# Performance work log

Hardware: AMD Instinct MI355X
Metric: run time of the kernel (lower is better)

## Reference

```python
import jax, jax.numpy as jnp
import numpy as np

N = 100000   # nodes
E = 1600000  # edges (edge_index1)
F_IN = 53    # num_features_xd
D1 = 128     # output_dim1
D2 = 64      # output_dim2
G = 512      # graphs in batch


def setup_inputs() -> dict:
    key = jax.random.key(0)
    ks = jax.random.split(key, 16)
    kaiming = lambda k, fi, fo: jax.random.normal(k, (fi, fo), jnp.float32) * np.float32(np.sqrt(2.0 / fi))
    glorot = lambda k, fi, fo: jax.random.normal(k, (fi, fo), jnp.float32) * np.float32(np.sqrt(1.0 / fi))
    return {
        "x": jax.random.normal(ks[0], (N, F_IN), jnp.float32),
        "edge_inter": jax.random.randint(ks[1], (2, E), 0, N),
        "edge_intra": jax.random.randint(ks[2], (2, E), 0, N),
        "batch": jnp.sort(jax.random.randint(ks[3], (N,), 0, G)),
        "num_graphs": G,
        "w1": kaiming(ks[4], F_IN, D1), "b1": jnp.zeros((D1,), jnp.float32),
        "w2": kaiming(ks[5], D1, D2), "b2": jnp.zeros((D2,), jnp.float32),
        "gat_w": glorot(ks[6], D2, D2),
        "att_src": jax.random.normal(ks[7], (D2,), jnp.float32) * 0.1,
        "att_dst": jax.random.normal(ks[8], (D2,), jnp.float32) * 0.1,
        "gat_b": jnp.zeros((D2,), jnp.float32),
        "gcn_w": glorot(ks[9], D2, 2 * D2), "gcn_b": jnp.zeros((2 * D2,), jnp.float32),
        "fc1_w": glorot(ks[10], 2 * D2, 512), "fc1_b": jnp.zeros((512,), jnp.float32),
        "fc2_w": glorot(ks[11], 512, 256), "fc2_b": jnp.zeros((256,), jnp.float32),
        "out_w": glorot(ks[12], 256, 1), "out_b": jnp.zeros((1,), jnp.float32),
    }


def reference(x, edge_inter, edge_intra, batch, num_graphs,
              w1, b1, w2, b2, gat_w, att_src, att_dst, gat_b,
              gcn_w, gcn_b, fc1_w, fc1_b, fc2_w, fc2_b, out_w, out_b):
    n = x.shape[0]
    # node_embed: two dense layers + relu
    h = jax.nn.relu(x @ w1 + b1)
    h = jax.nn.relu(h @ w2 + b2)

    # add self-loops (PyG default for GATConv and GCNConv)
    loops = jnp.arange(n)
    src = jnp.concatenate([edge_inter[0], loops])  # message source j
    dst = jnp.concatenate([edge_inter[1], loops])  # message target i

    # ---- GATConv (heads=1): gather -> score -> edge softmax -> scatter ----
    hp = h @ gat_w                           # [N, D2]
    a_s = hp @ att_src                       # [N]
    a_d = hp @ att_dst                       # [N]
    e = jax.nn.leaky_relu(a_s[src] + a_d[dst], negative_slope=0.2)  # [E+N]
    emax = jax.ops.segment_max(e, dst, num_segments=n)
    ee = jnp.exp(e - emax[dst])
    denom = jax.ops.segment_sum(ee, dst, num_segments=n)
    alpha = ee / denom[dst]                  # edge softmax per target node
    h = jax.ops.segment_sum(alpha[:, None] * hp[src], dst, num_segments=n) + gat_b
    h = jax.nn.relu(h)

    # ---- GCNConv: symmetric-normalized sparse aggregation ----
    hw = h @ gcn_w                           # [N, 2*D2]
    deg = jax.ops.segment_sum(jnp.ones_like(e), dst, num_segments=n)
    d_inv = jnp.where(deg > 0, deg ** -0.5, 0.0)
    norm = d_inv[src] * d_inv[dst]           # [E+N]
    h = jax.ops.segment_sum(norm[:, None] * hw[src], dst, num_segments=n) + gcn_b
    h = jax.nn.relu(h)

    # ---- global max pool over graphs ----
    g = jax.ops.segment_max(h, batch, num_segments=num_graphs)
    g = jnp.maximum(g, 0.0)  # guard empty segments (-inf); h >= 0 after relu

    # ---- MLP head (dropout is identity in eval mode) ----
    z = jax.nn.relu(g @ fc1_w + fc1_b)
    z = jax.nn.relu(z @ fc2_w + fc2_b)
    return z @ out_w + out_b
```

## Files before the change

### kernel.cpp

```cpp
#include <hip/hip_runtime.h>
#include <hip/hip_bf16.h>

#define F_IN 53
#define D1   128
#define D2   64
#define D3   128
#define H1SZ 512
#define H2SZ 256

#define BUKSZ   256
#define BUKMAX  512
#define CAP     5120
#define PART_CH 4096

__global__ void k_vecproj(const float* __restrict__ gat_w,
                          const float* __restrict__ att_src,
                          const float* __restrict__ att_dst,
                          float* __restrict__ v_src, float* __restrict__ v_dst) {
    int k = threadIdx.x;
    float as = 0.f, ad = 0.f;
    #pragma unroll
    for (int c = 0; c < D2; ++c) {
        float w = gat_w[k * D2 + c];
        as = fmaf(w, att_src[c], as);
        ad = fmaf(w, att_dst[c], ad);
    }
    v_src[k] = as;
    v_dst[k] = ad;
}

__global__ __launch_bounds__(256) void k_fused(const float* __restrict__ x,
                                               const float* __restrict__ w1,
                                               const float* __restrict__ b1,
                                               const float* __restrict__ w2,
                                               const float* __restrict__ b2,
                                               const float* __restrict__ gat_w,
                                               const float* __restrict__ v_src,
                                               const float* __restrict__ v_dst,
                                               float* __restrict__ hp,
                                               float* __restrict__ a_s,
                                               float* __restrict__ a_d,
                                               const int* __restrict__ ei,
                                               int* __restrict__ gcount,
                                               int2* __restrict__ tmp,
                                               const int* __restrict__ batch,
                                               int* __restrict__ gstart,
                                               int N, int E, int NBUK, int G,
                                               int embB, int partB) {
    __shared__ __align__(16) union {
        struct { float xs[32][56]; float h1s[32][D1]; float h2s[32][D2]; } e;
        int hist[BUKMAX];
    } sm;
    int tid = threadIdx.x;
    int bid = blockIdx.x;

    if (bid >= embB) {
        if (bid < embB + partB) {
            for (int i = tid; i < NBUK; i += 256) sm.hist[i] = 0;
            __syncthreads();
            int k0 = (bid - embB) * PART_CH;
            int ss[16], dd[16];
            #pragma unroll
            for (int i = 0; i < 16; ++i) {
                int k = k0 + i * 256 + tid;
                if (k < E) {
                    ss[i] = ei[k];
                    dd[i] = ei[E + k];
                    atomicAdd(&sm.hist[dd[i] >> 8], 1);
                } else {
                    dd[i] = -1;
                }
            }
            __syncthreads();
            for (int b = tid; b < NBUK; b += 256) {
                int c = sm.hist[b];
                if (c > 0) sm.hist[b] = b * CAP + atomicAdd(&gcount[b], c);
            }
            __syncthreads();
            #pragma unroll
            for (int i = 0; i < 16; ++i) {
                if (dd[i] >= 0) {
                    int b = dd[i] >> 8;
                    int pos = atomicAdd(&sm.hist[b], 1);
                    if (pos < (b + 1) * CAP) tmp[pos] = make_int2(ss[i], dd[i]);
                }
            }
        } else {
            int n = (bid - embB - partB) * 256 + tid;
            if (n < N) {
                int b = batch[n];
                if (n == 0) {
                    for (int g = 0; g <= b; ++g) gstart[g] = 0;
                } else {
                    int pb = batch[n - 1];
                    for (int g = pb + 1; g <= b; ++g) gstart[g] = n;
                }
                if (n == N - 1) {
                    for (int g = b + 1; g <= G; ++g) gstart[g] = N;
                }
            }
        }
        return;
    }

    int n0 = bid * 32;
    for (int i = tid; i < 32 * F_IN; i += 256) {
        int node = i / F_IN, kk = i - node * F_IN;
        sm.e.xs[node][kk] = x[(size_t)n0 * F_IN + i];
    }
    __syncthreads();
    int c = tid & 63, grp = tid >> 6;
    int nb = grp * 8;
    {
        float acc0[8], acc1[8];
        float bb0 = b1[c], bb1 = b1[c + 64];
        #pragma unroll
        for (int j = 0; j < 8; ++j) { acc0[j] = bb0; acc1[j] = bb1; }
        #pragma unroll 1
        for (int kc = 0; kc < 13; ++kc) {
            int k4 = kc * 4;
            float wa0 = w1[(k4 + 0) * D1 + c];
            float wa1 = w1[(k4 + 1) * D1 + c];
            float wa2 = w1[(k4 + 2) * D1 + c];
            float wa3 = w1[(k4 + 3) * D1 + c];
            float wb0 = w1[(k4 + 0) * D1 + c + 64];
            float wb1 = w1[(k4 + 1) * D1 + c + 64];
            float wb2 = w1[(k4 + 2) * D1 + c + 64];
            float wb3 = w1[(k4 + 3) * D1 + c + 64];
            #pragma unroll
            for (int j = 0; j < 8; ++j) {
                float4 xv = *reinterpret_cast<const float4*>(&sm.e.xs[nb + j][k4]);
                acc0[j] = fmaf(xv.x, wa0, acc0[j]);
                acc0[j] = fmaf(xv.y, wa1, acc0[j]);
                acc0[j] = fmaf(xv.z, wa2, acc0[j]);
                acc0[j] = fmaf(xv.w, wa3, acc0[j]);
                acc1[j] = fmaf(xv.x, wb0, acc1[j]);
                acc1[j] = fmaf(xv.y, wb1, acc1[j]);
                acc1[j] = fmaf(xv.z, wb2, acc1[j]);
                acc1[j] = fmaf(xv.w, wb3, acc1[j]);
            }
        }
        {
            float wa = w1[52 * D1 + c], wb = w1[52 * D1 + c + 64];
            #pragma unroll
            for (int j = 0; j < 8; ++j) {
                float xv = sm.e.xs[nb + j][52];
                acc0[j] = fmaf(xv, wa, acc0[j]);
                acc1[j] = fmaf(xv, wb, acc1[j]);
            }
        }
        #pragma unroll
        for (int j = 0; j < 8; ++j) {
            sm.e.h1s[nb + j][c]      = fmaxf(acc0[j], 0.f);
            sm.e.h1s[nb + j][c + 64] = fmaxf(acc1[j], 0.f);
        }
    }
    float h2v[8];
    {
        float bb = b2[c];
        #pragma unroll
        for (int j = 0; j < 8; ++j) h2v[j] = bb;
        #pragma unroll 1
        for (int kc = 0; kc < 32; ++kc) {
            int k4 = kc * 4;
            float w0 = w2[(k4 + 0) * D2 + c];
            float w1v = w2[(k4 + 1) * D2 + c];
            float w2v = w2[(k4 + 2) * D2 + c];
            float w3v = w2[(k4 + 3) * D2 + c];
            #pragma unroll
            for (int j = 0; j < 8; ++j) {
                float4 hv = *reinterpret_cast<const float4*>(&sm.e.h1s[nb + j][k4]);
                h2v[j] = fmaf(hv.x, w0, h2v[j]);
                h2v[j] = fmaf(hv.y, w1v, h2v[j]);
                h2v[j] = fmaf(hv.z, w2v, h2v[j]);
                h2v[j] = fmaf(hv.w, w3v, h2v[j]);
            }
        }
        #pragma unroll
        for (int j = 0; j < 8; ++j) {
            float v = fmaxf(h2v[j], 0.f);
            h2v[j] = v;
            sm.e.h2s[nb + j][c] = v;
        }
    }
    {
        float vs = v_src[c], vd = v_dst[c];
        #pragma unroll
        for (int j = 0; j < 8; ++j) {
            float ps = h2v[j] * vs, pd = h2v[j] * vd;
            #pragma unroll
            for (int off = 32; off; off >>= 1) {
                ps += __shfl_down(ps, off);
                pd += __shfl_down(pd, off);
            }
            if (c == 0) { int n = n0 + nb + j; a_s[n] = ps; a_d[n] = pd; }
        }
    }
    {
        float acc[8];
        #pragma unroll
        for (int j = 0; j < 8; ++j) acc[j] = 0.f;
        #pragma unroll 1
        for (int kc = 0; kc < 16; ++kc) {
            int k4 = kc * 4;
            float w0 = gat_w[(k4 + 0) * D2 + c];
            float w1v = gat_w[(k4 + 1) * D2 + c];
            float w2v = gat_w[(k4 + 2) * D2 + c];
            float w3v = gat_w[(k4 + 3) * D2 + c];
            #pragma unroll
            for (int j = 0; j < 8; ++j) {
                float4 hv = *reinterpret_cast<const float4*>(&sm.e.h2s[nb + j][k4]);
                acc[j] = fmaf(hv.x, w0, acc[j]);
                acc[j] = fmaf(hv.y, w1v, acc[j]);
                acc[j] = fmaf(hv.z, w2v, acc[j]);
                acc[j] = fmaf(hv.w, w3v, acc[j]);
            }
        }
        #pragma unroll
        for (int j = 0; j < 8; ++j)
            hp[(size_t)(n0 + nb + j) * D2 + c] = acc[j];
    }
}

__global__ __launch_bounds__(256) void k_build(const int2* __restrict__ tmp,
                                               const int* __restrict__ gcount,
                                               int* __restrict__ offs,
                                               int* __restrict__ degi,
                                               float* __restrict__ dinv,
                                               int* __restrict__ csr_src, int N) {
    __shared__ int ldeg[256];
    __shared__ int lsc[256];
    __shared__ int lcur[256];
    __shared__ int pref[256];
    int tid = threadIdx.x;
    int b = blockIdx.x;
    int n0 = b * BUKSZ;
    int nvalid = min(BUKSZ, N - n0);
    int cnt = min(gcount[b], CAP);
    int acc = 0;
    for (int i = tid; i < b; i += 256) acc += min(gcount[i], CAP);
    pref[tid] = acc;
    ldeg[tid] = 0;
    __syncthreads();
    #pragma unroll
    for (int off = 128; off; off >>= 1) {
        if (tid < off) pref[tid] += pref[tid + off];
        __syncthreads();
    }
    int base = pref[0] + n0;
    for (int i = tid; i < cnt; i += 256) {
        int2 e = tmp[b * CAP + i];
        atomicAdd(&ldeg[e.y & 255], 1);
    }
    __syncthreads();
    int d = (tid < nvalid) ? (ldeg[tid] + 1) : 0;
    lsc[tid] = d;
    __syncthreads();
    #pragma unroll
    for (int off = 1; off < 256; off <<= 1) {
        int u = (tid >= off) ? lsc[tid - off] : 0;
        __syncthreads();
        lsc[tid] += u;
        __syncthreads();
    }
    int excl = lsc[tid] - d;
    if (tid < nvalid) {
        int n = n0 + tid;
        offs[n] = base + excl;
        degi[n] = d;
        dinv[n] = rsqrtf((float)d);
        lcur[tid] = excl;
    }
    __syncthreads();
    for (int i = tid; i < cnt; i += 256) {
        int2 e = tmp[b * CAP + i];
        int nl = e.y & 255;
        int r = atomicAdd(&lcur[nl], 1);
        csr_src[base + r] = e.x;
    }
    __syncthreads();
    if (tid < nvalid) {
        int r = atomicAdd(&lcur[tid], 1);
        csr_src[base + r] = n0 + tid;
    }
}

__global__ __launch_bounds__(256) void k_gat(const int* __restrict__ csr_src,
                                             const int* __restrict__ offs,
                                             const int* __restrict__ degi,
                                             const float* __restrict__ a_s,
                                             const float* __restrict__ a_d,
                                             const float* __restrict__ hp,
                                             const float* __restrict__ gat_b,
                                             const float* __restrict__ dinv,
                                             float* __restrict__ hscaled, int N) {
    __shared__ float ac[4][128];
    int wv = threadIdx.x >> 6, lane = threadIdx.x & 63;
    int node = blockIdx.x * 4 + wv;
    if (node >= N) return;
    int start = offs[node], deg = degi[node];
    int dcap = min(deg, 128);
    float adn = a_d[node];
    float m = -1e30f, ssum = 0.f;
    for (int p = lane; p < deg; p += 64) {
        int s = csr_src[start + p];
        float e = a_s[s] + adn;
        e = (e > 0.f) ? e : 0.2f * e;
        if (p < 128) ac[wv][p] = e;
        float mn = fmaxf(m, e);
        ssum = ssum * __expf(m - mn) + __expf(e - mn);
        m = mn;
    }
    #pragma unroll
    for (int off = 32; off; off >>= 1) {
        float om = __shfl_xor(m, off);
        float os = __shfl_xor(ssum, off);
        float mn = fmaxf(m, om);
        ssum = ssum * __expf(m - mn) + os * __expf(om - mn);
        m = mn;
    }
    float rinv = 1.0f / ssum;
    if (lane < dcap)      ac[wv][lane]      = __expf(ac[wv][lane] - m) * rinv;
    if (lane + 64 < dcap) ac[wv][lane + 64] = __expf(ac[wv][lane + 64] - m) * rinv;
    float acc = 0.f;
    for (int pp = 0; pp < dcap; pp += 16) {
        int s[16]; float w[16];
        #pragma unroll
        for (int i = 0; i < 16; ++i) {
            int q = pp + i;
            int qc = (q < dcap) ? q : (dcap - 1);
            s[i] = csr_src[start + qc];
            w[i] = (q < dcap) ? ac[wv][q] : 0.f;
        }
        float v[16];
        #pragma unroll
        for (int i = 0; i < 16; ++i) v[i] = hp[(size_t)s[i] * D2 + lane];
        #pragma unroll
        for (int i = 0; i < 16; ++i) acc = fmaf(w[i], v[i], acc);
    }
    for (int p = 128; p < deg; ++p) {
        int s = csr_src[start + p];
        float e = a_s[s] + adn;
        e = (e > 0.f) ? e : 0.2f * e;
        acc = fmaf(__expf(e - m) * rinv, hp[(size_t)s * D2 + lane], acc);
    }
    hscaled[(size_t)node * D2 + lane] = dinv[node] * fmaxf(acc + gat_b[lane], 0.f);
}

__global__ __launch_bounds__(256) void k_gcn(const int* __restrict__ csr_src,
                                             const int* __restrict__ offs,
                                             const int* __restrict__ degi,
                                             const float* __restrict__ dinv,
                                             const float* __restrict__ hscaled,
                                             float* __restrict__ hagg, int N) {
    int node = blockIdx.x * 4 + (threadIdx.x >> 6);
    int lane = threadIdx.x & 63;
    if (node >= N) return;
    int start = offs[node], deg = degi[node];
    float acc = 0.f;
    for (int pp = 0; pp < deg; pp += 16) {
        int s[16];
        #pragma unroll
        for (int i = 0; i < 16; ++i) {
            int q = pp + i;
            int qc = (q < deg) ? q : (deg - 1);
            s[i] = csr_src[start + qc];
        }
        float v[16];
        #pragma unroll
        for (int i = 0; i < 16; ++i) v[i] = hscaled[(size_t)s[i] * D2 + lane];
        #pragma unroll
        for (int i = 0; i < 16; ++i) acc += (pp + i < deg) ? v[i] : 0.f;
    }
    hagg[(size_t)node * D2 + lane] = acc * dinv[node];
}

__global__ __launch_bounds__(512) void k_pool(const float* __restrict__ hagg,
                                              const float* __restrict__ gcn_w,
                                              const float* __restrict__ gcn_b,
                                              const int* __restrict__ gstart,
                                              float* __restrict__ g) {
    __shared__ float ws[D2 * D3];
    __shared__ __align__(16) float rows[16 * D2];
    __shared__ float red[512];
    int tid = threadIdx.x;
    int gi = blockIdx.x;
    for (int i = tid; i < D2 * D3; i += 512) ws[i] = gcn_w[i];
    int ns = gstart[gi], ne = gstart[gi + 1];
    int col = tid & 127, grp = tid >> 7;
    float bias = gcn_b[col];
    float runmax = 0.f;
    for (int base = ns; base < ne; base += 16) {
        int cnt = min(16, ne - base);
        __syncthreads();
        for (int i = tid; i < cnt * D2; i += 512)
            rows[i] = hagg[(size_t)base * D2 + i];
        __syncthreads();
        int nb = grp * 4;
        float a0 = bias, a1 = bias, a2 = bias, a3 = bias;
        #pragma unroll 4
        for (int kc = 0; kc < 16; ++kc) {
            int k4 = kc * 4;
            float w0 = ws[(k4 + 0) * D3 + col];
            float w1v = ws[(k4 + 1) * D3 + col];
            float w2v = ws[(k4 + 2) * D3 + col];
            float w3v = ws[(k4 + 3) * D3 + col];
            float4 r0 = *reinterpret_cast<const float4*>(&rows[(nb + 0) * D2 + k4]);
            float4 r1 = *reinterpret_cast<const float4*>(&rows[(nb + 1) * D2 + k4]);
            float4 r2 = *reinterpret_cast<const float4*>(&rows[(nb + 2) * D2 + k4]);
            float4 r3 = *reinterpret_cast<const float4*>(&rows[(nb + 3) * D2 + k4]);
            a0 = fmaf(r0.x, w0, a0); a0 = fmaf(r0.y, w1v, a0);
            a0 = fmaf(r0.z, w2v, a0); a0 = fmaf(r0.w, w3v, a0);
            a1 = fmaf(r1.x, w0, a1); a1 = fmaf(r1.y, w1v, a1);
            a1 = fmaf(r1.z, w2v, a1); a1 = fmaf(r1.w, w3v, a1);
            a2 = fmaf(r2.x, w0, a2); a2 = fmaf(r2.y, w1v, a2);
            a2 = fmaf(r2.z, w2v, a2); a2 = fmaf(r2.w, w3v, a2);
            a3 = fmaf(r3.x, w0, a3); a3 = fmaf(r3.y, w1v, a3);
            a3 = fmaf(r3.z, w2v, a3); a3 = fmaf(r3.w, w3v, a3);
        }
        if (nb + 0 < cnt) runmax = fmaxf(runmax, a0);
        if (nb + 1 < cnt) runmax = fmaxf(runmax, a1);
        if (nb + 2 < cnt) runmax = fmaxf(runmax, a2);
        if (nb + 3 < cnt) runmax = fmaxf(runmax, a3);
    }
    red[tid] = runmax;
    __syncthreads();
    if (tid < 128) {
        float v = fmaxf(fmaxf(red[tid], red[tid + 128]),
                        fmaxf(red[tid + 256], red[tid + 384]));
        g[(size_t)gi * D3 + tid] = v;
    }
}

__global__ __launch_bounds__(512) void k_fc1(const float* __restrict__ g,
                                             const float* __restrict__ w,
                                             const float* __restrict__ b,
                                             float* __restrict__ z1) {
    __shared__ float gs[4 * D3];
    int t = threadIdx.x;
    int g0 = blockIdx.x * 4;
    if (t < 4 * D3) gs[t] = g[(size_t)g0 * D3 + t];
    __syncthreads();
    float bias = b[t];
    float a0 = bias, a1 = bias, a2 = bias, a3 = bias;
    for (int k = 0; k < D3; ++k) {
        float wv = w[k * H1SZ + t];
        a0 = fmaf(gs[k], wv, a0);
        a1 = fmaf(gs[D3 + k], wv, a1);
        a2 = fmaf(gs[2 * D3 + k], wv, a2);
        a3 = fmaf(gs[3 * D3 + k], wv, a3);
    }
    z1[(size_t)(g0 + 0) * H1SZ + t] = fmaxf(a0, 0.f);
    z1[(size_t)(g0 + 1) * H1SZ + t] = fmaxf(a1, 0.f);
    z1[(size_t)(g0 + 2) * H1SZ + t] = fmaxf(a2, 0.f);
    z1[(size_t)(g0 + 3) * H1SZ + t] = fmaxf(a3, 0.f);
}

__global__ __launch_bounds__(256) void k_fc2(const float* __restrict__ z1,
                                             const float* __restrict__ w,
                                             const float* __restrict__ b,
                                             float* __restrict__ z2) {
    __shared__ float zs[4 * H1SZ];
    int t = threadIdx.x;
    int g0 = blockIdx.x * 4;
    for (int i = t; i < 4 * H1SZ; i += 256) zs[i] = z1[(size_t)g0 * H1SZ + i];
    __syncthreads();
    float bias = b[t];
    float a0 = bias, a1 = bias, a2 = bias, a3 = bias;
    for (int k = 0; k < H1SZ; ++k) {
        float wv = w[k * H2SZ + t];
        a0 = fmaf(zs[k], wv, a0);
        a1 = fmaf(zs[H1SZ + k], wv, a1);
        a2 = fmaf(zs[2 * H1SZ + k], wv, a2);
        a3 = fmaf(zs[3 * H1SZ + k], wv, a3);
    }
    z2[(size_t)(g0 + 0) * H2SZ + t] = fmaxf(a0, 0.f);
    z2[(size_t)(g0 + 1) * H2SZ + t] = fmaxf(a1, 0.f);
    z2[(size_t)(g0 + 2) * H2SZ + t] = fmaxf(a2, 0.f);
    z2[(size_t)(g0 + 3) * H2SZ + t] = fmaxf(a3, 0.f);
}

__global__ __launch_bounds__(256) void k_out(const float* __restrict__ z2,
                                             const float* __restrict__ out_w,
                                             const float* __restrict__ out_b,
                                             float* __restrict__ out) {
    __shared__ float red[4];
    int gi = blockIdx.x, t = threadIdx.x;
    float p = z2[(size_t)gi * H2SZ + t] * out_w[t];
    #pragma unroll
    for (int off = 32; off; off >>= 1) p += __shfl_down(p, off);
    int lane = t & 63, w = t >> 6;
    if (lane == 0) red[w] = p;
    __syncthreads();
    if (t == 0) out[gi] = red[0] + red[1] + red[2] + red[3] + out_b[0];
}

extern "C" void kernel_launch(void* const* d_in, const int* in_sizes, int n_in,
                              void* d_out, int out_size, void* d_ws, size_t ws_size,
                              hipStream_t stream) {
    const float* x        = (const float*)d_in[0];
    const int*   ei       = (const int*)d_in[1];
    const int*   batch    = (const int*)d_in[3];
    const float* w1       = (const float*)d_in[5];
    const float* b1       = (const float*)d_in[6];
    const float* w2       = (const float*)d_in[7];
    const float* b2       = (const float*)d_in[8];
    const float* gat_w    = (const float*)d_in[9];
    const float* att_src  = (const float*)d_in[10];
    const float* att_dst  = (const float*)d_in[11];
    const float* gat_b    = (const float*)d_in[12];
    const float* gcn_w    = (const float*)d_in[13];
    const float* gcn_b    = (const float*)d_in[14];
    const float* fc1_w    = (const float*)d_in[15];
    const float* fc1_b    = (const float*)d_in[16];
    const float* fc2_w    = (const float*)d_in[17];
    const float* fc2_b    = (const float*)d_in[18];
    const float* out_w    = (const float*)d_in[19];
    const float* out_b    = (const float*)d_in[20];
    float* out = (float*)d_out;

    const int N = in_sizes[0] / F_IN;
    const int E = in_sizes[1] / 2;
    const int M = E + N;
    const int G = out_size;
    const int NBUK = (N + BUKSZ - 1) / BUKSZ;
    const int embB   = N / 32;
    const int partB  = (E + PART_CH - 1) / PART_CH;
    const int boundB = (N + 255) / 256;

    char* p = (char*)d_ws;
    size_t off = 0;
    auto alloc = [&](size_t bytes) { void* q = p + off; off += (bytes + 255) & ~(size_t)255; return q; };
    int2*  tmp     = (int2*)alloc((size_t)NBUK * CAP * 8);
    int*   csr_src = (int*)alloc((size_t)M * 4);
    float* hp      = (float*)alloc((size_t)N * D2 * 4);
    float* hscaled = (float*)alloc((size_t)N * D2 * 4);
    float* hagg    = (float*)alloc((size_t)N * D2 * 4);
    int*   offs    = (int*)alloc((size_t)N * 4);
    int*   degi    = (int*)alloc((size_t)N * 4);
    float* dinv    = (float*)alloc((size_t)N * 4);
    float* a_s     = (float*)alloc((size_t)N * 4);
    float* a_d     = (float*)alloc((size_t)N * 4);
    int*   gcount  = (int*)alloc((size_t)NBUK * 4);
    int*   gstart  = (int*)alloc((size_t)(G + 1) * 4);
    float* g       = (float*)alloc((size_t)G * D3 * 4);
    float* z1      = (float*)alloc((size_t)G * H1SZ * 4);
    float* z2      = (float*)alloc((size_t)G * H2SZ * 4);
    float* v_src   = (float*)alloc(D2 * 4);
    float* v_dst   = (float*)alloc(D2 * 4);

    hipMemsetAsync(gcount, 0, (size_t)NBUK * 4, stream);

    k_vecproj<<<1, 64, 0, stream>>>(gat_w, att_src, att_dst, v_src, v_dst);
    k_fused<<<embB + partB + boundB, 256, 0, stream>>>(
        x, w1, b1, w2, b2, gat_w, v_src, v_dst, hp, a_s, a_d,
        ei, gcount, tmp, batch, gstart, N, E, NBUK, G, embB, partB);
    k_build<<<NBUK, 256, 0, stream>>>(tmp, gcount, offs, degi, dinv, csr_src, N);
    k_gat<<<(N + 3) / 4, 256, 0, stream>>>(csr_src, offs, degi, a_s, a_d, hp,
                                           gat_b, dinv, hscaled, N);
    k_gcn<<<(N + 3) / 4, 256, 0, stream>>>(csr_src, offs, degi, dinv, hscaled, hagg, N);
    k_pool<<<G, 512, 0, stream>>>(hagg, gcn_w, gcn_b, gstart, g);
    k_fc1<<<G / 4, 512, 0, stream>>>(g, fc1_w, fc1_b, z1);
    k_fc2<<<G / 4, 256, 0, stream>>>(z1, fc2_w, fc2_b, z2);
    k_out<<<G, 256, 0, stream>>>(z2, out_w, out_b, out);
}
```

Before: 345.0 us.

## Fuse GCN aggregation into per-graph pooling kernel with double-buffered rows

Merges the GCN neighbour-gather kernel into the pooling kernel, so each graph's block gathers 8 node rows per step into shared memory. That step's 128-column transform and max-pool run while the next 8 rows are gathered into a second buffer. This drops the N x 64 hagg intermediate and its write and read round trip, plus one launch. It also lets the x-tile and h2 buffers share one shared-memory array in the embedding kernel. The risk is that the gather, about 1.7M edges, now runs on only 512 blocks, one per graph, which may leave the GPU underoccupied compared with the previous 25k-block gather.

```diff
diff --git a/kernel.cpp b/kernel.cpp
--- a/kernel.cpp
+++ b/kernel.cpp
@@ -48,7 +48,7 @@
                                                int N, int E, int NBUK, int G,
                                                int embB, int partB) {
     __shared__ __align__(16) union {
-        struct { float xs[32][56]; float h1s[32][D1]; float h2s[32][D2]; } e;
+        struct { float buf[32][64]; float h1s[32][D1]; } e;
         int hist[BUKMAX];
     } sm;
     int tid = threadIdx.x;
@@ -106,7 +106,7 @@
     int n0 = bid * 32;
     for (int i = tid; i < 32 * F_IN; i += 256) {
         int node = i / F_IN, kk = i - node * F_IN;
-        sm.e.xs[node][kk] = x[(size_t)n0 * F_IN + i];
+        sm.e.buf[node][kk] = x[(size_t)n0 * F_IN + i];
     }
     __syncthreads();
     int c = tid & 63, grp = tid >> 6;
@@ -129,7 +129,7 @@
             float wb3 = w1[(k4 + 3) * D1 + c + 64];
             #pragma unroll
             for (int j = 0; j < 8; ++j) {
-                float4 xv = *reinterpret_cast<const float4*>(&sm.e.xs[nb + j][k4]);
+                float4 xv = *reinterpret_cast<const float4*>(&sm.e.buf[nb + j][k4]);
                 acc0[j] = fmaf(xv.x, wa0, acc0[j]);
                 acc0[j] = fmaf(xv.y, wa1, acc0[j]);
                 acc0[j] = fmaf(xv.z, wa2, acc0[j]);
@@ -144,7 +144,7 @@
             float wa = w1[52 * D1 + c], wb = w1[52 * D1 + c + 64];
             #pragma unroll
             for (int j = 0; j < 8; ++j) {
-                float xv = sm.e.xs[nb + j][52];
+                float xv = sm.e.buf[nb + j][52];
                 acc0[j] = fmaf(xv, wa, acc0[j]);
                 acc1[j] = fmaf(xv, wb, acc1[j]);
             }
@@ -180,7 +180,7 @@
         for (int j = 0; j < 8; ++j) {
             float v = fmaxf(h2v[j], 0.f);
             h2v[j] = v;
-            sm.e.h2s[nb + j][c] = v;
+            sm.e.buf[nb + j][c] = v;
         }
     }
     {
@@ -209,7 +209,7 @@
             float w3v = gat_w[(k4 + 3) * D2 + c];
             #pragma unroll
             for (int j = 0; j < 8; ++j) {
-                float4 hv = *reinterpret_cast<const float4*>(&sm.e.h2s[nb + j][k4]);
+                float4 hv = *reinterpret_cast<const float4*>(&sm.e.buf[nb + j][k4]);
                 acc[j] = fmaf(hv.x, w0, acc[j]);
                 acc[j] = fmaf(hv.y, w1v, acc[j]);
                 acc[j] = fmaf(hv.z, w2v, acc[j]);
@@ -347,57 +347,57 @@
     hscaled[(size_t)node * D2 + lane] = dinv[node] * fmaxf(acc + gat_b[lane], 0.f);
 }
 
-__global__ __launch_bounds__(256) void k_gcn(const int* __restrict__ csr_src,
-                                             const int* __restrict__ offs,
-                                             const int* __restrict__ degi,
-                                             const float* __restrict__ dinv,
-                                             const float* __restrict__ hscaled,
-                                             float* __restrict__ hagg, int N) {
-    int node = blockIdx.x * 4 + (threadIdx.x >> 6);
-    int lane = threadIdx.x & 63;
-    if (node >= N) return;
-    int start = offs[node], deg = degi[node];
-    float acc = 0.f;
-    for (int pp = 0; pp < deg; pp += 16) {
-        int s[16];
-        #pragma unroll
-        for (int i = 0; i < 16; ++i) {
-            int q = pp + i;
-            int qc = (q < deg) ? q : (deg - 1);
-            s[i] = csr_src[start + qc];
-        }
-        float v[16];
-        #pragma unroll
-        for (int i = 0; i < 16; ++i) v[i] = hscaled[(size_t)s[i] * D2 + lane];
-        #pragma unroll
-        for (int i = 0; i < 16; ++i) acc += (pp + i < deg) ? v[i] : 0.f;
-    }
-    hagg[(size_t)node * D2 + lane] = acc * dinv[node];
-}
-
-__global__ __launch_bounds__(512) void k_pool(const float* __restrict__ hagg,
-                                              const float* __restrict__ gcn_w,
-                                              const float* __restrict__ gcn_b,
-                                              const int* __restrict__ gstart,
-                                              float* __restrict__ g) {
+__global__ __launch_bounds__(512) void k_gcnpool(const int* __restrict__ csr_src,
+                                                 const int* __restrict__ offs,
+                                                 const int* __restrict__ degi,
+                                                 const float* __restrict__ dinv,
+                                                 const float* __restrict__ hscaled,
+                                                 const float* __restrict__ gcn_w,
+                                                 const float* __restrict__ gcn_b,
+                                                 const int* __restrict__ gstart,
+                                                 float* __restrict__ g) {
     __shared__ float ws[D2 * D3];
-    __shared__ __align__(16) float rows[16 * D2];
+    __shared__ __align__(16) float rows[2][8][D2];
     __shared__ float red[512];
     int tid = threadIdx.x;
     int gi = blockIdx.x;
     for (int i = tid; i < D2 * D3; i += 512) ws[i] = gcn_w[i];
     int ns = gstart[gi], ne = gstart[gi + 1];
+    int wv = tid >> 6, lane = tid & 63;
     int col = tid & 127, grp = tid >> 7;
     float bias = gcn_b[col];
     float runmax = 0.f;
-    for (int base = ns; base < ne; base += 16) {
-        int cnt = min(16, ne - base);
-        __syncthreads();
-        for (int i = tid; i < cnt * D2; i += 512)
-            rows[i] = hagg[(size_t)base * D2 + i];
-        __syncthreads();
-        int nb = grp * 4;
-        float a0 = bias, a1 = bias, a2 = bias, a3 = bias;
+
+    auto gather = [&](int base, int sel) {
+        int node = base + wv;
+        if (node < ne) {
+            int start = offs[node], deg = degi[node];
+            float acc = 0.f;
+            for (int pp = 0; pp < deg; pp += 16) {
+                int s[16];
+                #pragma unroll
+                for (int i = 0; i < 16; ++i) {
+                    int q = pp + i;
+                    int qc = (q < deg) ? q : (deg - 1);
+                    s[i] = csr_src[start + qc];
+                }
+                float v[16];
+                #pragma unroll
+                for (int i = 0; i < 16; ++i) v[i] = hscaled[(size_t)s[i] * D2 + lane];
+                #pragma unroll
+                for (int i = 0; i < 16; ++i) acc += (pp + i < deg) ? v[i] : 0.f;
+            }
+            rows[sel][wv][lane] = acc * dinv[node];
+        }
+    };
+
+    if (ns < ne) gather(ns, 0);
+    __syncthreads();
+    for (int base = ns; base < ne; base += 8) {
+        int cur = ((base - ns) >> 3) & 1;
+        if (base + 8 < ne) gather(base + 8, cur ^ 1);
+        int nb = grp * 2;
+        float a0 = bias, a1 = bias;
         #pragma unroll 4
         for (int kc = 0; kc < 16; ++kc) {
             int k4 = kc * 4;
@@ -405,23 +405,16 @@
             float w1v = ws[(k4 + 1) * D3 + col];
             float w2v = ws[(k4 + 2) * D3 + col];
             float w3v = ws[(k4 + 3) * D3 + col];
-            float4 r0 = *reinterpret_cast<const float4*>(&rows[(nb + 0) * D2 + k4]);
-            float4 r1 = *reinterpret_cast<const float4*>(&rows[(nb + 1) * D2 + k4]);
-            float4 r2 = *reinterpret_cast<const float4*>(&rows[(nb + 2) * D2 + k4]);
-            float4 r3 = *reinterpret_cast<const float4*>(&rows[(nb + 3) * D2 + k4]);
+            float4 r0 = *reinterpret_cast<const float4*>(&rows[cur][nb][k4]);
+            float4 r1 = *reinterpret_cast<const float4*>(&rows[cur][nb + 1][k4]);
             a0 = fmaf(r0.x, w0, a0); a0 = fmaf(r0.y, w1v, a0);
             a0 = fmaf(r0.z, w2v, a0); a0 = fmaf(r0.w, w3v, a0);
             a1 = fmaf(r1.x, w0, a1); a1 = fmaf(r1.y, w1v, a1);
             a1 = fmaf(r1.z, w2v, a1); a1 = fmaf(r1.w, w3v, a1);
-            a2 = fmaf(r2.x, w0, a2); a2 = fmaf(r2.y, w1v, a2);
-            a2 = fmaf(r2.z, w2v, a2); a2 = fmaf(r2.w, w3v, a2);
-            a3 = fmaf(r3.x, w0, a3); a3 = fmaf(r3.y, w1v, a3);
-            a3 = fmaf(r3.z, w2v, a3); a3 = fmaf(r3.w, w3v, a3);
-        }
-        if (nb + 0 < cnt) runmax = fmaxf(runmax, a0);
-        if (nb + 1 < cnt) runmax = fmaxf(runmax, a1);
-        if (nb + 2 < cnt) runmax = fmaxf(runmax, a2);
-        if (nb + 3 < cnt) runmax = fmaxf(runmax, a3);
+        }
+        if (base + nb < ne)     runmax = fmaxf(runmax, a0);
+        if (base + nb + 1 < ne) runmax = fmaxf(runmax, a1);
+        __syncthreads();
     }
     red[tid] = runmax;
     __syncthreads();
@@ -535,7 +528,6 @@
     int*   csr_src = (int*)alloc((size_t)M * 4);
     float* hp      = (float*)alloc((size_t)N * D2 * 4);
     float* hscaled = (float*)alloc((size_t)N * D2 * 4);
-    float* hagg    = (float*)alloc((size_t)N * D2 * 4);
     int*   offs    = (int*)alloc((size_t)N * 4);
     int*   degi    = (int*)alloc((size_t)N * 4);
     float* dinv    = (float*)alloc((size_t)N * 4);
@@ -558,8 +550,8 @@
     k_build<<<NBUK, 256, 0, stream>>>(tmp, gcount, offs, degi, dinv, csr_src, N);
     k_gat<<<(N + 3) / 4, 256, 0, stream>>>(csr_src, offs, degi, a_s, a_d, hp,
                                            gat_b, dinv, hscaled, N);
-    k_gcn<<<(N + 3) / 4, 256, 0, stream>>>(csr_src, offs, degi, dinv, hscaled, hagg, N);
-    k_pool<<<G, 512, 0, stream>>>(hagg, gcn_w, gcn_b, gstart, g);
+    k_gcnpool<<<G, 512, 0, stream>>>(csr_src, offs, degi, dinv, hscaled,
+                                     gcn_w, gcn_b, gstart, g);
     k_fc1<<<G / 4, 512, 0, stream>>>(g, fc1_w, fc1_b, z1);
     k_fc2<<<G / 4, 256, 0, stream>>>(z1, fc2_w, fc2_b, z2);
     k_out<<<G, 256, 0, stream>>>(z2, out_w, out_b, out);
```

After: 351.7 us. Within noise of the previous version (+1.9%).
